# Kernel tuning notes

Measured on AMD Instinct MI355X. Metric: run time of the kernel, lower is better.

The kernel has to match this reference:

```python
import jax, jax.numpy as jnp
import numpy as np

B, F, H, W = 2, 8, 16, 16
S = F * H * W                 # 2048 tokens
DIM, NH = 2048, 16
HD = DIM // NH                # 128
C = HD // 2                   # 64 complex pairs per head
CT = C - 2 * (C // 3)         # 22 temporal freqs
CH = C // 3                   # 21 height / 21 width freqs
L = 1024                      # freq table length
SHIFT = 4                     # TCROPE_SHIFT
EPS = 1e-6


def setup_inputs():
    key = jax.random.key(0)
    ks = jax.random.split(key, 12)
    lin = lambda k: jax.random.normal(k, (DIM, DIM), jnp.float32) / np.sqrt(DIM)
    x = jax.random.normal(ks[0], (B, S, DIM), jnp.float32)
    q_w, k_w, v_w, o_w = lin(ks[1]), lin(ks[2]), lin(ks[3]), lin(ks[4])
    q_b = jax.random.normal(ks[5], (DIM,), jnp.float32) * 0.02
    k_b = jax.random.normal(ks[6], (DIM,), jnp.float32) * 0.02
    v_b = jax.random.normal(ks[7], (DIM,), jnp.float32) * 0.02
    o_b = jax.random.normal(ks[8], (DIM,), jnp.float32) * 0.02
    norm_q_w = jnp.ones((DIM,), jnp.float32)
    norm_k_w = jnp.ones((DIM,), jnp.float32)
    # unit-magnitude complex rotations stored as (cos, sin): [L, C, 2]
    inv = 1.0 / (10000.0 ** (np.arange(C, dtype=np.float32) / C))
    ang = np.arange(L, dtype=np.float32)[:, None] * inv[None, :]
    freqs = jnp.asarray(np.stack([np.cos(ang), np.sin(ang)], axis=-1))
    seq_lens = jnp.full((B,), S, jnp.int32)
    grid_sizes = jnp.tile(jnp.array([[F, H, W]], jnp.int32), (B, 1))
    inner_t = jnp.array([[4, 4], [3, 5]], jnp.int32)  # per-sample shot lengths, sum == F
    return dict(x=x, q_w=q_w, q_b=q_b, k_w=k_w, k_b=k_b, v_w=v_w, v_b=v_b,
                o_w=o_w, o_b=o_b, norm_q_w=norm_q_w, norm_k_w=norm_k_w,
                freqs=freqs, seq_lens=seq_lens, grid_sizes=grid_sizes, inner_t=inner_t)


def _rmsnorm(x, w):
    return x * jax.lax.rsqrt(jnp.mean(x * x, axis=-1, keepdims=True) + EPS) * w


def _rope(x, freqs, inner_t, seq_lens):
    # x: [B,S,NH,HD]; per-sample 3D RoPE over (f,h,w) with per-shot temporal index shift.
    xr = x.reshape(B, S, NH, C, 2)
    f0, f1, f2 = freqs[:, :CT], freqs[:, CT:CT + CH], freqs[:, CT + CH:]
    t = jnp.arange(F)
    # frame t belongs to shot j  =>  temporal freq index = j*SHIFT + t  (matches freq_select)
    shot = jax.vmap(lambda it: jnp.searchsorted(jnp.cumsum(it), t, side='right'))(inner_t)
    t_idx = shot * SHIFT + t[None, :]                                   # [B,F]
    tf = jnp.broadcast_to(f0[t_idx][:, :, None, None], (B, F, H, W, CT, 2))
    hf = jnp.broadcast_to(f1[:H][None, None, :, None], (B, F, H, W, CH, 2))
    wf = jnp.broadcast_to(f2[:W][None, None, None, :], (B, F, H, W, CH, 2))
    fr = jnp.concatenate([tf, hf, wf], axis=-2).reshape(B, S, 1, C, 2)  # [B,S,1,C,2]
    a, b = xr[..., 0], xr[..., 1]
    cr, ci = fr[..., 0], fr[..., 1]
    rot = jnp.stack([a * cr - b * ci, a * ci + b * cr], axis=-1).reshape(B, S, NH, HD)
    # positions past f*h*w are left un-rotated in the original (tail concat)
    keep = (jnp.arange(S)[None, :] < seq_lens[:, None])[:, :, None, None]
    return jnp.where(keep, rot, x)


def reference(x, q_w, q_b, k_w, k_b, v_w, v_b, o_w, o_b,
              norm_q_w, norm_k_w, freqs, seq_lens, grid_sizes, inner_t):
    # grid_sizes is (F,H,W) for every sample; baked in as static constants above.
    q = _rmsnorm(x @ q_w + q_b, norm_q_w).reshape(B, S, NH, HD)
    k = _rmsnorm(x @ k_w + k_b, norm_k_w).reshape(B, S, NH, HD)
    v = (x @ v_w + v_b).reshape(B, S, NH, HD)
    q = _rope(q, freqs, inner_t, seq_lens)
    k = _rope(k, freqs, inner_t, seq_lens)
    scores = jnp.einsum('bqnd,bknd->bnqk', q, k) * (HD ** -0.5)
    kmask = (jnp.arange(S)[None, :] < seq_lens[:, None])[:, None, None, :]
    scores = jnp.where(kmask, scores, -1e30)
    attn = jax.nn.softmax(scores, axis=-1)
    out = jnp.einsum('bnqk,bknd->bqnd', attn, v).reshape(B, S, DIM)
    return out @ o_w + o_b
```

## Files before the change

kernel.cpp:

```cpp
#include <hip/hip_runtime.h>


typedef __attribute__((ext_vector_type(8))) short bf16x8;
typedef __attribute__((ext_vector_type(4))) float f32x4;

__device__ __forceinline__ unsigned short f2bf(float f) {
  unsigned int u = __builtin_bit_cast(unsigned int, f);
  u = (u + 0x7FFFu + ((u >> 16) & 1u)) >> 16;
  return (unsigned short)u;
}
__device__ __forceinline__ float bf2f(unsigned short h) {
  unsigned int u = ((unsigned int)h) << 16;
  return __builtin_bit_cast(float, u);
}

#define GLOAD16(gp, lp)                                                        \
  __builtin_amdgcn_global_load_lds(                                            \
      (__attribute__((address_space(1))) void*)(gp),                           \
      (__attribute__((address_space(3))) void*)(lp), 16, 0, 0)

__global__ __launch_bounds__(256) void k_prep(const float* __restrict__ x,
                                              unsigned short* __restrict__ xb,
                                              const float* __restrict__ qw,
                                              const float* __restrict__ kw,
                                              const float* __restrict__ vw,
                                              const float* __restrict__ ow,
                                              unsigned short* __restrict__ qkT,
                                              unsigned short* __restrict__ vT,
                                              unsigned short* __restrict__ oT) {
  const int bid = blockIdx.x;
  const int tid = threadIdx.x;
  if (bid >= 4096) {
    const int i = (bid - 4096) * 256 + tid;
    const float4* p = (const float4*)x + (size_t)i * 2;
    float4 a = p[0], b = p[1];
    bf16x8 v;
    v[0] = (short)f2bf(a.x); v[1] = (short)f2bf(a.y);
    v[2] = (short)f2bf(a.z); v[3] = (short)f2bf(a.w);
    v[4] = (short)f2bf(b.x); v[5] = (short)f2bf(b.y);
    v[6] = (short)f2bf(b.z); v[7] = (short)f2bf(b.w);
    *(bf16x8*)(xb + (size_t)i * 8) = v;
    return;
  }
  __shared__ float tile[64][65];
  const int mat = bid >> 10, t10 = bid & 1023;
  const float* in = (mat == 0) ? qw : (mat == 1) ? kw : (mat == 2) ? vw : ow;
  unsigned short* out = (mat == 0) ? qkT
                      : (mat == 1) ? (qkT + (size_t)2048 * 2048)
                      : (mat == 2) ? vT : oT;
  const int r0 = (t10 >> 5) * 64, c0 = (t10 & 31) * 64;
#pragma unroll
  for (int i = 0; i < 4; i++) {
    const int fi = tid + i * 256;
    const int row = fi >> 4, c4 = fi & 15;
    float4 v = *(const float4*)(in + (size_t)(r0 + row) * 2048 + c0 + c4 * 4);
    tile[row][c4 * 4 + 0] = v.x; tile[row][c4 * 4 + 1] = v.y;
    tile[row][c4 * 4 + 2] = v.z; tile[row][c4 * 4 + 3] = v.w;
  }
  __syncthreads();
#pragma unroll
  for (int i = 0; i < 2; i++) {
    const int oi = tid + i * 256;
    const int c = oi >> 3, r8 = oi & 7;
    bf16x8 o;
#pragma unroll
    for (int j = 0; j < 8; j++) o[j] = (short)f2bf(tile[r8 * 8 + j][c]);
    *(bf16x8*)(out + (size_t)(c0 + c) * 2048 + r0 + r8 * 8) = o;
  }
}

template <int OUTF32, int BIASMODE>
__global__ __launch_bounds__(256) void k_gemm(const unsigned short* __restrict__ A,
                                              const unsigned short* __restrict__ BT,
                                              void* __restrict__ Cout,
                                              const float* __restrict__ bias,
                                              int M, int N, int K) {
  __shared__ unsigned short As[128 * 32];
  __shared__ unsigned short Bs[128 * 32];
  const int tid = threadIdx.x;
  const int lane = tid & 63, w = tid >> 6;
  const int g = lane >> 4, cc = lane & 15;
  const int gx = gridDim.x;
  int id = blockIdx.y * gx + blockIdx.x;
  const int tot = gx * gridDim.y;
  id = (id & 7) * (tot >> 3) + (id >> 3);
  const int n0 = (id % gx) * 128, m0 = (id / gx) * 128;
  const int wm = (w >> 1) * 64, wn = (w & 1) * 64;
  f32x4 acc[4][4] = {};
  const unsigned short* Ab = A + (size_t)m0 * K;
  const unsigned short* Bb = BT + (size_t)n0 * K;
  const int r0 = tid >> 2, c0 = (tid & 3) * 8;
  for (int kt = 0; kt < K; kt += 32) {
    GLOAD16(Ab + (size_t)r0 * K + kt + c0, As + tid * 8);
    GLOAD16(Ab + (size_t)(r0 + 64) * K + kt + c0, As + (tid + 256) * 8);
    GLOAD16(Bb + (size_t)r0 * K + kt + c0, Bs + tid * 8);
    GLOAD16(Bb + (size_t)(r0 + 64) * K + kt + c0, Bs + (tid + 256) * 8);
    __syncthreads();
    bf16x8 af[4], bfr[4];
#pragma unroll
    for (int m4 = 0; m4 < 4; m4++)
      af[m4] = *(const bf16x8*)(As + (wm + m4 * 16 + cc) * 32 + g * 8);
#pragma unroll
    for (int n4 = 0; n4 < 4; n4++)
      bfr[n4] = *(const bf16x8*)(Bs + (wn + n4 * 16 + cc) * 32 + g * 8);
#pragma unroll
    for (int m4 = 0; m4 < 4; m4++)
#pragma unroll
      for (int n4 = 0; n4 < 4; n4++)
        acc[m4][n4] = __builtin_amdgcn_mfma_f32_16x16x32_bf16(af[m4], bfr[n4],
                                                              acc[m4][n4], 0, 0, 0);
    __syncthreads();
  }
#pragma unroll
  for (int m4 = 0; m4 < 4; m4++)
#pragma unroll
    for (int n4 = 0; n4 < 4; n4++) {
      const int col = n0 + wn + n4 * 16 + cc;
#pragma unroll
      for (int r = 0; r < 4; r++) {
        const int row = m0 + wm + m4 * 16 + g * 4 + r;
        float v = acc[m4][n4][r];
        if (BIASMODE == 1) v += bias[row];
        if (BIASMODE == 2) v += bias[col];
        if (OUTF32)
          ((float*)Cout)[(size_t)row * N + col] = v;
        else
          ((unsigned short*)Cout)[(size_t)row * N + col] = f2bf(v);
      }
    }
}

__device__ __forceinline__ void stage_half(const unsigned short* __restrict__ src,
                                           int K, unsigned short* dst, int tid) {
#pragma unroll
  for (int j = 0; j < 2; j++) {
    const int li = tid + j * 512;
    const int r = li >> 3;
    const int c16 = (li & 7) ^ (r & 7);
    GLOAD16(src + (size_t)r * K + c16 * 8, (char*)dst + li * 16);
  }
}

__global__ __launch_bounds__(512, 2) void k_gemm_yqk(const unsigned short* __restrict__ A,
                                                     const unsigned short* __restrict__ BT,
                                                     unsigned short* __restrict__ Cout) {
  __shared__ unsigned short As[2][256 * 64];
  __shared__ unsigned short Bs[2][256 * 64];
  const int tid = threadIdx.x;
  const int lane = tid & 63, w = tid >> 6;
  const int g = lane >> 4, cc = lane & 15;
  const int wm = (w >> 2) * 128, wn = (w & 3) * 64;
  const int swz = (cc & 7) << 4;
  const int N = 4096, K = 2048;
  int id = blockIdx.x;
  id = (id & 7) * 32 + (id >> 3);
  const int m0 = (id >> 4) * 256, n0 = (id & 15) * 256;
  f32x4 acc[8][4] = {};
  const int T = K >> 6;

  stage_half(BT + (size_t)n0 * K, K, Bs[0], tid);
  stage_half(A + (size_t)m0 * K, K, As[0], tid);
  stage_half(BT + (size_t)(n0 + 128) * K, K, Bs[0] + 8192, tid);
  stage_half(A + (size_t)(m0 + 128) * K, K, As[0] + 8192, tid);
  stage_half(BT + (size_t)n0 * K + 64, K, Bs[1], tid);
  stage_half(A + (size_t)m0 * K + 64, K, As[1], tid);
  asm volatile("s_waitcnt vmcnt(4)" ::: "memory");
  __builtin_amdgcn_s_barrier();

  for (int t = 0; t < T; ++t) {
    const int c = t & 1;
    const char* Ac = (const char*)As[c];
    const char* Bc = (const char*)Bs[c];
    bf16x8 ar[4][2], br[4][2];
#pragma unroll
    for (int m = 0; m < 4; m++)
#pragma unroll
      for (int kk = 0; kk < 2; kk++)
        ar[m][kk] = *(const bf16x8*)(Ac + (wm + m * 16 + cc) * 128 +
                                     ((kk * 64 + g * 16) ^ swz));
#pragma unroll
    for (int n = 0; n < 2; n++)
#pragma unroll
      for (int kk = 0; kk < 2; kk++)
        br[n][kk] = *(const bf16x8*)(Bc + (wn + n * 16 + cc) * 128 +
                                     ((kk * 64 + g * 16) ^ swz));
    stage_half(BT + (size_t)(n0 + 128) * K + ((t + 1) & (T - 1)) * 64, K,
               Bs[c ^ 1] + 8192, tid);
    __builtin_amdgcn_s_barrier();
    __builtin_amdgcn_sched_barrier(0);
    __builtin_amdgcn_s_setprio(1);
#pragma unroll
    for (int kk = 0; kk < 2; kk++)
#pragma unroll
      for (int m = 0; m < 4; m++)
#pragma unroll
        for (int n = 0; n < 2; n++)
          acc[m][n] = __builtin_amdgcn_mfma_f32_16x16x32_bf16(ar[m][kk], br[n][kk],
                                                              acc[m][n], 0, 0, 0);
    __builtin_amdgcn_s_setprio(0);
    __builtin_amdgcn_s_barrier();
    __builtin_amdgcn_sched_barrier(0);
#pragma unroll
    for (int n = 2; n < 4; n++)
#pragma unroll
      for (int kk = 0; kk < 2; kk++)
        br[n][kk] = *(const bf16x8*)(Bc + (wn + n * 16 + cc) * 128 +
                                     ((kk * 64 + g * 16) ^ swz));
    stage_half(A + (size_t)(m0 + 128) * K + ((t + 1) & (T - 1)) * 64, K,
               As[c ^ 1] + 8192, tid);
    __builtin_amdgcn_s_barrier();
    __builtin_amdgcn_sched_barrier(0);
    __builtin_amdgcn_s_setprio(1);
#pragma unroll
    for (int kk = 0; kk < 2; kk++)
#pragma unroll
      for (int m = 0; m < 4; m++)
#pragma unroll
        for (int n = 2; n < 4; n++)
          acc[m][n] = __builtin_amdgcn_mfma_f32_16x16x32_bf16(ar[m][kk], br[n][kk],
                                                              acc[m][n], 0, 0, 0);
    __builtin_amdgcn_s_setprio(0);
    __builtin_amdgcn_s_barrier();
    __builtin_amdgcn_sched_barrier(0);
#pragma unroll
    for (int m = 0; m < 4; m++)
#pragma unroll
      for (int kk = 0; kk < 2; kk++)
        ar[m][kk] = *(const bf16x8*)(Ac + (wm + (m + 4) * 16 + cc) * 128 +
                                     ((kk * 64 + g * 16) ^ swz));
    stage_half(BT + (size_t)n0 * K + ((t + 2) & (T - 1)) * 64, K, Bs[c], tid);
    __builtin_amdgcn_s_barrier();
    __builtin_amdgcn_sched_barrier(0);
    __builtin_amdgcn_s_setprio(1);
#pragma unroll
    for (int kk = 0; kk < 2; kk++)
#pragma unroll
      for (int m = 0; m < 4; m++)
#pragma unroll
        for (int n = 0; n < 2; n++)
          acc[m + 4][n] = __builtin_amdgcn_mfma_f32_16x16x32_bf16(ar[m][kk], br[n][kk],
                                                                  acc[m + 4][n], 0, 0, 0);
    __builtin_amdgcn_s_setprio(0);
    __builtin_amdgcn_s_barrier();
    __builtin_amdgcn_sched_barrier(0);
    stage_half(A + (size_t)m0 * K + ((t + 2) & (T - 1)) * 64, K, As[c], tid);
    __builtin_amdgcn_s_setprio(1);
#pragma unroll
    for (int kk = 0; kk < 2; kk++)
#pragma unroll
      for (int m = 0; m < 4; m++)
#pragma unroll
        for (int n = 2; n < 4; n++)
          acc[m + 4][n] = __builtin_amdgcn_mfma_f32_16x16x32_bf16(ar[m][kk], br[n][kk],
                                                                  acc[m + 4][n], 0, 0, 0);
    __builtin_amdgcn_s_setprio(0);
    if (t < T - 2)
      asm volatile("s_waitcnt vmcnt(4)" ::: "memory");
    else
      asm volatile("s_waitcnt vmcnt(0)" ::: "memory");
    __builtin_amdgcn_sched_barrier(0);
    __builtin_amdgcn_s_barrier();
    __builtin_amdgcn_sched_barrier(0);
  }

#pragma unroll
  for (int mi = 0; mi < 8; mi++)
#pragma unroll
    for (int n = 0; n < 4; n++) {
      const int col = n0 + wn + n * 16 + cc;
#pragma unroll
      for (int j = 0; j < 4; j++) {
        const int row = m0 + wm + mi * 16 + g * 4 + j;
        Cout[(size_t)row * N + col] = f2bf(acc[mi][n][j]);
      }
    }
}

__global__ __launch_bounds__(256) void k_qk_epi(const unsigned short* __restrict__ Yqk,
                                                const float* __restrict__ q_b,
                                                const float* __restrict__ k_b,
                                                const float* __restrict__ nqw,
                                                const float* __restrict__ nkw,
                                                const float* __restrict__ freqs,
                                                const int* __restrict__ inner_t,
                                                unsigned short* __restrict__ Q,
                                                unsigned short* __restrict__ K) {
  const int row = blockIdx.x;
  const int b = row >> 11, s = row & 2047;
  const int t = threadIdx.x;
  const unsigned short* yr = Yqk + (size_t)row * 4096;
  bf16x8 yq = *(const bf16x8*)(yr + t * 8);
  bf16x8 yk = *(const bf16x8*)(yr + 2048 + t * 8);
  float4 qb0 = *(const float4*)(q_b + t * 8), qb1 = *(const float4*)(q_b + t * 8 + 4);
  float4 kb0 = *(const float4*)(k_b + t * 8), kb1 = *(const float4*)(k_b + t * 8 + 4);
  float q[8], k[8];
  q[0] = bf2f((unsigned short)yq[0]) + qb0.x; q[1] = bf2f((unsigned short)yq[1]) + qb0.y;
  q[2] = bf2f((unsigned short)yq[2]) + qb0.z; q[3] = bf2f((unsigned short)yq[3]) + qb0.w;
  q[4] = bf2f((unsigned short)yq[4]) + qb1.x; q[5] = bf2f((unsigned short)yq[5]) + qb1.y;
  q[6] = bf2f((unsigned short)yq[6]) + qb1.z; q[7] = bf2f((unsigned short)yq[7]) + qb1.w;
  k[0] = bf2f((unsigned short)yk[0]) + kb0.x; k[1] = bf2f((unsigned short)yk[1]) + kb0.y;
  k[2] = bf2f((unsigned short)yk[2]) + kb0.z; k[3] = bf2f((unsigned short)yk[3]) + kb0.w;
  k[4] = bf2f((unsigned short)yk[4]) + kb1.x; k[5] = bf2f((unsigned short)yk[5]) + kb1.y;
  k[6] = bf2f((unsigned short)yk[6]) + kb1.z; k[7] = bf2f((unsigned short)yk[7]) + kb1.w;
  float ssq = 0.f, ssk = 0.f;
#pragma unroll
  for (int j = 0; j < 8; j++) { ssq += q[j] * q[j]; ssk += k[j] * k[j]; }
#pragma unroll
  for (int off = 32; off; off >>= 1) {
    ssq += __shfl_xor(ssq, off);
    ssk += __shfl_xor(ssk, off);
  }
  __shared__ float red[8];
  const int w = t >> 6;
  if ((t & 63) == 0) { red[w] = ssq; red[4 + w] = ssk; }
  __syncthreads();
  const float sq = red[0] + red[1] + red[2] + red[3];
  const float sk = red[4] + red[5] + red[6] + red[7];
  const float rq = __builtin_amdgcn_rsqf(sq * (1.0f / 2048.0f) + 1e-6f);
  const float rk = __builtin_amdgcn_rsqf(sk * (1.0f / 2048.0f) + 1e-6f);
  float4 nq0 = *(const float4*)(nqw + t * 8), nq1 = *(const float4*)(nqw + t * 8 + 4);
  float4 nk0 = *(const float4*)(nkw + t * 8), nk1 = *(const float4*)(nkw + t * 8 + 4);
  q[0] *= rq * nq0.x; q[1] *= rq * nq0.y; q[2] *= rq * nq0.z; q[3] *= rq * nq0.w;
  q[4] *= rq * nq1.x; q[5] *= rq * nq1.y; q[6] *= rq * nq1.z; q[7] *= rq * nq1.w;
  k[0] *= rk * nk0.x; k[1] *= rk * nk0.y; k[2] *= rk * nk0.z; k[3] *= rk * nk0.w;
  k[4] *= rk * nk1.x; k[5] *= rk * nk1.y; k[6] *= rk * nk1.z; k[7] *= rk * nk1.w;
  const int f = s >> 8, hh = (s >> 4) & 15, ww = s & 15;
  const int it0 = inner_t[b * 2], it1 = inner_t[b * 2 + 1];
  const int trow = ((f >= it0) + (f >= it0 + it1)) * 4 + f;
#pragma unroll
  for (int jj = 0; jj < 4; jj++) {
    const int c = (t * 4 + jj) & 63;
    const int fr = (c < 22) ? trow : ((c < 43) ? hh : ww);
    const float cr = freqs[((size_t)fr * 64 + c) * 2];
    const float ci = freqs[((size_t)fr * 64 + c) * 2 + 1];
    float a = q[2 * jj], bb = q[2 * jj + 1];
    q[2 * jj] = a * cr - bb * ci; q[2 * jj + 1] = a * ci + bb * cr;
    a = k[2 * jj]; bb = k[2 * jj + 1];
    k[2 * jj] = a * cr - bb * ci; k[2 * jj + 1] = a * ci + bb * cr;
  }
  const float QSCALE = 0.08838834764831845f * 1.4426950408889634f;
  bf16x8 oq, ok;
#pragma unroll
  for (int j = 0; j < 8; j++) {
    oq[j] = (short)f2bf(q[j] * QSCALE);
    ok[j] = (short)f2bf(k[j]);
  }
  const int head = t >> 4, d0 = (t & 15) * 8;
  const size_t off = ((size_t)(b * 16 + head) * 2048 + s) * 128 + d0;
  *(bf16x8*)(Q + off) = oq;
  *(bf16x8*)(K + off) = ok;
}

__global__ __launch_bounds__(512, 4) void k_attn(const unsigned short* __restrict__ Q,
                                                 const unsigned short* __restrict__ K,
                                                 const unsigned short* __restrict__ V,
                                                 unsigned short* __restrict__ O) {
  __shared__ unsigned short Ks[2][64 * 128];
  __shared__ unsigned short Vs[2][128 * 64];
  __shared__ unsigned short Ps[8 * 16 * 64];
  const int tid = threadIdx.x;
  const int lane = tid & 63, w = tid >> 6;
  const int g = lane >> 4, cc = lane & 15;
  const int orig = blockIdx.x;
  const int lid = (orig & 7) * 64 + (orig >> 3);
  const int bh = lid >> 4;
  const int q0 = (lid & 15) * 128;
  const int b = bh >> 4, h = bh & 15;

  const unsigned short* Qb = Q + ((size_t)bh * 2048 + q0 + w * 16 + cc) * 128;
  bf16x8 qf[4];
#pragma unroll
  for (int kk = 0; kk < 4; kk++) qf[kk] = *(const bf16x8*)(Qb + kk * 32 + g * 8);

  const char* kbase = (const char*)(K + (size_t)bh * 2048 * 128);
  const char* vbase = (const char*)V + ((size_t)h * 128 * 4096 + (size_t)b * 2048) * 2;

  f32x4 acc[8] = {};
  float mloc = -3.0e38f, lloc = 0.f;
  char* Pb = (char*)Ps + w * 2048 + cc * 128;
  const int psw = (cc & 7) << 4;
  const int gbase = (lane & 48) | (((lane >> 4) & 3) << 2);
  const f32x4 vzero = {0.f, 0.f, 0.f, 0.f};

#define ATTN_STAGE(s0, bi)                                                     \
  {                                                                            \
    const char* kt0 = kbase + (size_t)(s0) * 256;                              \
    const char* vt0 = vbase + (size_t)(s0) * 2;                                \
    char* Kd = (char*)(Ks[bi]);                                                \
    char* Vd = (char*)(Vs[bi]);                                                \
    _Pragma("unroll") for (int i = 0; i < 2; i++) {                            \
      const int li = i * 512 + tid;                                            \
      const int kr = li >> 4;                                                  \
      const int kc = ((li & 15) * 16) ^ ((kr & 7) << 4);                       \
      GLOAD16(kt0 + kr * 256 + kc, Kd + li * 16);                              \
      const int vd = li >> 3;                                                  \
      const int vc = ((li & 7) * 16) ^ ((vd & 7) << 4);                        \
      GLOAD16(vt0 + (size_t)vd * 8192 + vc, Vd + li * 16);                     \
    }                                                                          \
  }

  ATTN_STAGE(0, 0);
  for (int t = 0; t < 32; ++t) {
    const int cur = t & 1;
    if (t < 31) {
      ATTN_STAGE((t + 1) * 64, cur ^ 1);
      asm volatile("s_waitcnt vmcnt(4)" ::: "memory");
    } else {
      asm volatile("s_waitcnt vmcnt(0)" ::: "memory");
    }
    __builtin_amdgcn_sched_barrier(0);
    __builtin_amdgcn_s_barrier();

    const char* kcur = (const char*)(Ks[cur]);
    const int sw = (cc & 7) << 4;
    f32x4 sf[4] = {vzero, vzero, vzero, vzero};
    __builtin_amdgcn_s_setprio(1);
#pragma unroll
    for (int kk = 0; kk < 4; kk++) {
      const int ko = (kk * 64 + g * 16) ^ sw;
      bf16x8 kf0 = *(const bf16x8*)(kcur + (cc)*256 + ko);
      bf16x8 kf1 = *(const bf16x8*)(kcur + (16 + cc) * 256 + ko);
      bf16x8 kf2 = *(const bf16x8*)(kcur + (32 + cc) * 256 + ko);
      bf16x8 kf3 = *(const bf16x8*)(kcur + (48 + cc) * 256 + ko);
      sf[0] = __builtin_amdgcn_mfma_f32_16x16x32_bf16(kf0, qf[kk], sf[0], 0, 0, 0);
      sf[1] = __builtin_amdgcn_mfma_f32_16x16x32_bf16(kf1, qf[kk], sf[1], 0, 0, 0);
      sf[2] = __builtin_amdgcn_mfma_f32_16x16x32_bf16(kf2, qf[kk], sf[2], 0, 0, 0);
      sf[3] = __builtin_amdgcn_mfma_f32_16x16x32_bf16(kf3, qf[kk], sf[3], 0, 0, 0);
    }
    __builtin_amdgcn_s_setprio(0);

    float tm = fmaxf(fmaxf(fmaxf(sf[0][0], sf[0][1]), fmaxf(sf[0][2], sf[0][3])),
                     fmaxf(fmaxf(sf[1][0], sf[1][1]), fmaxf(sf[1][2], sf[1][3])));
    tm = fmaxf(tm, fmaxf(fmaxf(fmaxf(sf[2][0], sf[2][1]), fmaxf(sf[2][2], sf[2][3])),
                         fmaxf(fmaxf(sf[3][0], sf[3][1]), fmaxf(sf[3][2], sf[3][3]))));
    tm = fmaxf(tm, __shfl_xor(tm, 16));
    tm = fmaxf(tm, __shfl_xor(tm, 32));
    if (__any(tm > mloc + 8.0f)) {
      const float mn = fmaxf(mloc, tm);
      const float sc = __builtin_amdgcn_exp2f(mloc - mn);
      mloc = mn;
      lloc *= sc;
      f32x4 scv;
#pragma unroll
      for (int r = 0; r < 4; r++) scv[r] = __shfl(sc, gbase + r);
#pragma unroll
      for (int d4 = 0; d4 < 8; d4++) acc[d4] *= scv;
    }
    float rs = 0.f;
#pragma unroll
    for (int n4 = 0; n4 < 4; n4++) {
      const float p0 = __builtin_amdgcn_exp2f(sf[n4][0] - mloc);
      const float p1 = __builtin_amdgcn_exp2f(sf[n4][1] - mloc);
      const float p2 = __builtin_amdgcn_exp2f(sf[n4][2] - mloc);
      const float p3 = __builtin_amdgcn_exp2f(sf[n4][3] - mloc);
      rs += (p0 + p1) + (p2 + p3);
      unsigned lo, hi;
      asm("v_cvt_pk_bf16_f32 %0, %1, %2" : "=v"(lo) : "v"(p0), "v"(p1));
      asm("v_cvt_pk_bf16_f32 %0, %1, %2" : "=v"(hi) : "v"(p2), "v"(p3));
      uint2 pv_; pv_.x = lo; pv_.y = hi;
      *(uint2*)(Pb + ((n4 * 32 + g * 8) ^ psw)) = pv_;
    }
    rs += __shfl_xor(rs, 16);
    rs += __shfl_xor(rs, 32);
    lloc += rs;

    const char* vcur = (const char*)(Vs[cur]);
    __builtin_amdgcn_s_setprio(1);
#pragma unroll
    for (int ks = 0; ks < 2; ks++) {
      bf16x8 pf = *(const bf16x8*)(Pb + ((ks * 64 + g * 16) ^ psw));
#pragma unroll
      for (int d4 = 0; d4 < 8; d4++) {
        const int dd = d4 * 16 + cc;
        bf16x8 vf = *(const bf16x8*)(vcur + dd * 128 +
                                     ((ks * 64 + g * 16) ^ ((dd & 7) << 4)));
        acc[d4] = __builtin_amdgcn_mfma_f32_16x16x32_bf16(pf, vf, acc[d4], 0, 0, 0);
      }
    }
    __builtin_amdgcn_s_setprio(0);

    asm volatile("s_waitcnt lgkmcnt(0)" ::: "memory");
    __builtin_amdgcn_sched_barrier(0);
    __builtin_amdgcn_s_barrier();
  }
#undef ATTN_STAGE

  const float invl = __builtin_amdgcn_rcpf(lloc);
  float ir[4];
#pragma unroll
  for (int r = 0; r < 4; r++) ir[r] = __shfl(invl, gbase + r);
  unsigned short* Ob = O + (size_t)(b * 2048 + q0 + w * 16) * 2048 + h * 128;
#pragma unroll
  for (int d4 = 0; d4 < 8; d4++)
#pragma unroll
    for (int r = 0; r < 4; r++)
      Ob[(size_t)(g * 4 + r) * 2048 + d4 * 16 + cc] = f2bf(acc[d4][r] * ir[r]);
}

extern "C" void kernel_launch(void* const* d_in, const int* in_sizes, int n_in,
                              void* d_out, int out_size, void* d_ws, size_t ws_size,
                              hipStream_t stream) {
  const float* x     = (const float*)d_in[0];
  const float* q_w   = (const float*)d_in[1];
  const float* q_b   = (const float*)d_in[2];
  const float* k_w   = (const float*)d_in[3];
  const float* k_b   = (const float*)d_in[4];
  const float* v_w   = (const float*)d_in[5];
  const float* v_b   = (const float*)d_in[6];
  const float* o_w   = (const float*)d_in[7];
  const float* o_b   = (const float*)d_in[8];
  const float* nqw   = (const float*)d_in[9];
  const float* nkw   = (const float*)d_in[10];
  const float* freqs = (const float*)d_in[11];
  const int* inner_t = (const int*)d_in[14];

  const size_t NEED = (size_t)112 << 20;
  if (ws_size < NEED) return;

  char* ws = (char*)d_ws;
  unsigned short* xb   = (unsigned short*)(ws);
  unsigned short* WqkT = (unsigned short*)(ws + ((size_t)16 << 20));
  unsigned short* WvT  = (unsigned short*)(ws + ((size_t)32 << 20));
  unsigned short* WoT  = (unsigned short*)(ws + ((size_t)40 << 20));
  unsigned short* Yqk  = (unsigned short*)(ws + ((size_t)48 << 20));
  unsigned short* Vt   = (unsigned short*)(ws + ((size_t)80 << 20));
  unsigned short* Kr   = (unsigned short*)(ws + ((size_t)96 << 20));
  unsigned short* Qr   = xb;
  unsigned short* Orow = WqkT;

  k_prep<<<8192, 256, 0, stream>>>(x, xb, q_w, k_w, v_w, o_w, WqkT, WvT, WoT);
  k_gemm_yqk<<<256, 512, 0, stream>>>(xb, WqkT, Yqk);
  k_gemm<0, 1><<<dim3(32, 16), 256, 0, stream>>>(WvT, xb, Vt, v_b, 2048, 4096, 2048);
  k_qk_epi<<<4096, 256, 0, stream>>>(Yqk, q_b, k_b, nqw, nkw, freqs, inner_t, Qr, Kr);
  k_attn<<<512, 512, 0, stream>>>(Qr, Kr, Vt, Orow);
  k_gemm<1, 2><<<dim3(16, 32), 256, 0, stream>>>(Orow, WoT, (float*)d_out, o_b, 4096, 2048, 2048);
}
```

Measured before the change: 313.2 us.

## Replace simple GEMMs for V and output projections with pipelined 256x128 tile kernel

Drops the basic 128x128 single-buffer GEMM used for the V projection and the output projection. Both now use a new 512-thread kernel with 256x128 tiles, double-buffered swizzled LDS, async global-to-LDS staging interleaved with MFMA phases, and s_setprio scheduling, modelled on the existing QK GEMM. The aim is to overlap memory loads with matrix math and raise reuse per tile. In exchange the grid drops to 256 blocks and each block needs much more LDS.

```diff
diff --git a/kernel.cpp b/kernel.cpp
--- a/kernel.cpp
+++ b/kernel.cpp
@@ -69,67 +69,6 @@
   }
 }
 
-template <int OUTF32, int BIASMODE>
-__global__ __launch_bounds__(256) void k_gemm(const unsigned short* __restrict__ A,
-                                              const unsigned short* __restrict__ BT,
-                                              void* __restrict__ Cout,
-                                              const float* __restrict__ bias,
-                                              int M, int N, int K) {
-  __shared__ unsigned short As[128 * 32];
-  __shared__ unsigned short Bs[128 * 32];
-  const int tid = threadIdx.x;
-  const int lane = tid & 63, w = tid >> 6;
-  const int g = lane >> 4, cc = lane & 15;
-  const int gx = gridDim.x;
-  int id = blockIdx.y * gx + blockIdx.x;
-  const int tot = gx * gridDim.y;
-  id = (id & 7) * (tot >> 3) + (id >> 3);
-  const int n0 = (id % gx) * 128, m0 = (id / gx) * 128;
-  const int wm = (w >> 1) * 64, wn = (w & 1) * 64;
-  f32x4 acc[4][4] = {};
-  const unsigned short* Ab = A + (size_t)m0 * K;
-  const unsigned short* Bb = BT + (size_t)n0 * K;
-  const int r0 = tid >> 2, c0 = (tid & 3) * 8;
-  for (int kt = 0; kt < K; kt += 32) {
-    GLOAD16(Ab + (size_t)r0 * K + kt + c0, As + tid * 8);
-    GLOAD16(Ab + (size_t)(r0 + 64) * K + kt + c0, As + (tid + 256) * 8);
-    GLOAD16(Bb + (size_t)r0 * K + kt + c0, Bs + tid * 8);
-    GLOAD16(Bb + (size_t)(r0 + 64) * K + kt + c0, Bs + (tid + 256) * 8);
-    __syncthreads();
-    bf16x8 af[4], bfr[4];
-#pragma unroll
-    for (int m4 = 0; m4 < 4; m4++)
-      af[m4] = *(const bf16x8*)(As + (wm + m4 * 16 + cc) * 32 + g * 8);
-#pragma unroll
-    for (int n4 = 0; n4 < 4; n4++)
-      bfr[n4] = *(const bf16x8*)(Bs + (wn + n4 * 16 + cc) * 32 + g * 8);
-#pragma unroll
-    for (int m4 = 0; m4 < 4; m4++)
-#pragma unroll
-      for (int n4 = 0; n4 < 4; n4++)
-        acc[m4][n4] = __builtin_amdgcn_mfma_f32_16x16x32_bf16(af[m4], bfr[n4],
-                                                              acc[m4][n4], 0, 0, 0);
-    __syncthreads();
-  }
-#pragma unroll
-  for (int m4 = 0; m4 < 4; m4++)
-#pragma unroll
-    for (int n4 = 0; n4 < 4; n4++) {
-      const int col = n0 + wn + n4 * 16 + cc;
-#pragma unroll
-      for (int r = 0; r < 4; r++) {
-        const int row = m0 + wm + m4 * 16 + g * 4 + r;
-        float v = acc[m4][n4][r];
-        if (BIASMODE == 1) v += bias[row];
-        if (BIASMODE == 2) v += bias[col];
-        if (OUTF32)
-          ((float*)Cout)[(size_t)row * N + col] = v;
-        else
-          ((unsigned short*)Cout)[(size_t)row * N + col] = f2bf(v);
-      }
-    }
-}
-
 __device__ __forceinline__ void stage_half(const unsigned short* __restrict__ src,
                                            int K, unsigned short* dst, int tid) {
 #pragma unroll
@@ -272,6 +211,133 @@
       for (int j = 0; j < 4; j++) {
         const int row = m0 + wm + mi * 16 + g * 4 + j;
         Cout[(size_t)row * N + col] = f2bf(acc[mi][n][j]);
+      }
+    }
+}
+
+template <int OUTF32, int BIASROW>
+__global__ __launch_bounds__(512, 2) void k_gemm_n128(const unsigned short* __restrict__ A,
+                                                      const unsigned short* __restrict__ BT,
+                                                      void* __restrict__ Cout,
+                                                      const float* __restrict__ bias,
+                                                      int N, int K) {
+  __shared__ unsigned short As[2][256 * 64];
+  __shared__ unsigned short Bs[2][128 * 64];
+  const int tid = threadIdx.x;
+  const int lane = tid & 63, w = tid >> 6;
+  const int g = lane >> 4, cc = lane & 15;
+  const int wm = (w >> 2) * 128, wn = (w & 3) * 32;
+  const int swz = (cc & 7) << 4;
+  const int nbx = N >> 7;
+  int id = blockIdx.x;
+  id = (id & 7) * 32 + (id >> 3);
+  const int m0 = (id / nbx) * 256, n0 = (id % nbx) * 128;
+  f32x4 acc[8][2] = {};
+  const int T = K >> 6;
+
+  stage_half(A + (size_t)m0 * K, K, As[0], tid);
+  stage_half(BT + (size_t)n0 * K, K, Bs[0], tid);
+  stage_half(A + (size_t)(m0 + 128) * K, K, As[0] + 8192, tid);
+  stage_half(A + (size_t)m0 * K + 64, K, As[1], tid);
+  asm volatile("s_waitcnt vmcnt(2)" ::: "memory");
+  __builtin_amdgcn_s_barrier();
+
+  for (int t = 0; t < T; ++t) {
+    const int c = t & 1;
+    const char* Ac = (const char*)As[c];
+    const char* Bc = (const char*)Bs[c];
+    bf16x8 ar[4][2], br[2][2];
+#pragma unroll
+    for (int m = 0; m < 4; m++)
+#pragma unroll
+      for (int kk = 0; kk < 2; kk++)
+        ar[m][kk] = *(const bf16x8*)(Ac + (wm + m * 16 + cc) * 128 +
+                                     ((kk * 64 + g * 16) ^ swz));
+#pragma unroll
+    for (int kk = 0; kk < 2; kk++)
+      br[0][kk] = *(const bf16x8*)(Bc + (wn + cc) * 128 +
+                                   ((kk * 64 + g * 16) ^ swz));
+    stage_half(BT + (size_t)n0 * K + ((t + 1) & (T - 1)) * 64, K, Bs[c ^ 1], tid);
+    __builtin_amdgcn_s_barrier();
+    __builtin_amdgcn_sched_barrier(0);
+    __builtin_amdgcn_s_setprio(1);
+#pragma unroll
+    for (int kk = 0; kk < 2; kk++)
+#pragma unroll
+      for (int m = 0; m < 4; m++)
+        acc[m][0] = __builtin_amdgcn_mfma_f32_16x16x32_bf16(ar[m][kk], br[0][kk],
+                                                            acc[m][0], 0, 0, 0);
+    __builtin_amdgcn_s_setprio(0);
+    __builtin_amdgcn_s_barrier();
+    __builtin_amdgcn_sched_barrier(0);
+#pragma unroll
+    for (int kk = 0; kk < 2; kk++)
+      br[1][kk] = *(const bf16x8*)(Bc + (wn + 16 + cc) * 128 +
+                                   ((kk * 64 + g * 16) ^ swz));
+    stage_half(A + (size_t)(m0 + 128) * K + ((t + 1) & (T - 1)) * 64, K,
+               As[c ^ 1] + 8192, tid);
+    __builtin_amdgcn_s_barrier();
+    __builtin_amdgcn_sched_barrier(0);
+    __builtin_amdgcn_s_setprio(1);
+#pragma unroll
+    for (int kk = 0; kk < 2; kk++)
+#pragma unroll
+      for (int m = 0; m < 4; m++)
+        acc[m][1] = __builtin_amdgcn_mfma_f32_16x16x32_bf16(ar[m][kk], br[1][kk],
+                                                            acc[m][1], 0, 0, 0);
+    __builtin_amdgcn_s_setprio(0);
+    __builtin_amdgcn_s_barrier();
+    __builtin_amdgcn_sched_barrier(0);
+#pragma unroll
+    for (int m = 0; m < 4; m++)
+#pragma unroll
+      for (int kk = 0; kk < 2; kk++)
+        ar[m][kk] = *(const bf16x8*)(Ac + (wm + (m + 4) * 16 + cc) * 128 +
+                                     ((kk * 64 + g * 16) ^ swz));
+    __builtin_amdgcn_s_barrier();
+    __builtin_amdgcn_sched_barrier(0);
+    __builtin_amdgcn_s_setprio(1);
+#pragma unroll
+    for (int kk = 0; kk < 2; kk++)
+#pragma unroll
+      for (int m = 0; m < 4; m++)
+        acc[m + 4][0] = __builtin_amdgcn_mfma_f32_16x16x32_bf16(ar[m][kk], br[0][kk],
+                                                                acc[m + 4][0], 0, 0, 0);
+    __builtin_amdgcn_s_setprio(0);
+    __builtin_amdgcn_s_barrier();
+    __builtin_amdgcn_sched_barrier(0);
+    stage_half(A + (size_t)m0 * K + ((t + 2) & (T - 1)) * 64, K, As[c], tid);
+    __builtin_amdgcn_s_setprio(1);
+#pragma unroll
+    for (int kk = 0; kk < 2; kk++)
+#pragma unroll
+      for (int m = 0; m < 4; m++)
+        acc[m + 4][1] = __builtin_amdgcn_mfma_f32_16x16x32_bf16(ar[m][kk], br[1][kk],
+                                                                acc[m + 4][1], 0, 0, 0);
+    __builtin_amdgcn_s_setprio(0);
+    if (t < T - 2)
+      asm volatile("s_waitcnt vmcnt(2)" ::: "memory");
+    else
+      asm volatile("s_waitcnt vmcnt(0)" ::: "memory");
+    __builtin_amdgcn_sched_barrier(0);
+    __builtin_amdgcn_s_barrier();
+    __builtin_amdgcn_sched_barrier(0);
+  }
+
+#pragma unroll
+  for (int mi = 0; mi < 8; mi++)
+#pragma unroll
+    for (int n = 0; n < 2; n++) {
+      const int col = n0 + wn + n * 16 + cc;
+#pragma unroll
+      for (int j = 0; j < 4; j++) {
+        const int row = m0 + wm + mi * 16 + g * 4 + j;
+        float v = acc[mi][n][j];
+        if (bias) v += BIASROW ? bias[row] : bias[col];
+        if (OUTF32)
+          ((float*)Cout)[(size_t)row * N + col] = v;
+        else
+          ((unsigned short*)Cout)[(size_t)row * N + col] = f2bf(v);
       }
     }
 }
@@ -530,8 +596,8 @@
 
   k_prep<<<8192, 256, 0, stream>>>(x, xb, q_w, k_w, v_w, o_w, WqkT, WvT, WoT);
   k_gemm_yqk<<<256, 512, 0, stream>>>(xb, WqkT, Yqk);
-  k_gemm<0, 1><<<dim3(32, 16), 256, 0, stream>>>(WvT, xb, Vt, v_b, 2048, 4096, 2048);
+  k_gemm_n128<0, 1><<<256, 512, 0, stream>>>(WvT, xb, Vt, v_b, 4096, 2048);
   k_qk_epi<<<4096, 256, 0, stream>>>(Yqk, q_b, k_b, nqw, nkw, freqs, inner_t, Qr, Kr);
   k_attn<<<512, 512, 0, stream>>>(Qr, Kr, Vt, Orow);
-  k_gemm<1, 2><<<dim3(16, 32), 256, 0, stream>>>(Orow, WoT, (float*)d_out, o_b, 4096, 2048, 2048);
-}
+  k_gemm_n128<1, 0><<<256, 512, 0, stream>>>(Orow, WoT, (float*)d_out, o_b, 2048, 2048);
+}
```

Result: slower. 331.0 us (+5.7%).
